# Kernel tuning notes

Hardware: AMD Instinct MI355X
Metric: run time of the kernel (lower is better)

The kernel has to match this reference:

```python
import jax, jax.numpy as jnp
import numpy as np

TOP_K = 10


def setup_inputs() -> dict:
    key = jax.random.key(0)
    x = jax.random.normal(key, (256, 1, 8192), dtype=jnp.float32)
    return {"x": x}


def reference(x):
    # x: [B, 1, S] real
    B, _, S = x.shape
    # torch.arange(1e-05, 1, 1/S) has exactly S elements for these S
    t = 1e-05 + jnp.arange(S, dtype=jnp.float32) / S            # [S]
    dft = jnp.fft.fft(x[:, 0, :], n=S, axis=-1, norm='ortho')   # [B, S] complex64
    mag = jnp.abs(dft)                                          # [B, S]
    top_idx = jnp.argsort(-mag, axis=-1)[:, :TOP_K]             # [B, k] int
    top_dft = jnp.take_along_axis(dft, top_idx, axis=1)         # [B, k] complex
    # complex exponential basis exp(-2j*pi*k*t), flipped along time
    phase = (-2j * jnp.pi) * (top_idx[:, :, None].astype(jnp.float32) * t[None, None, :])
    bs = jnp.exp(phase)[:, :, ::-1]                             # [B, k, S] complex
    bf = top_dft[:, :, None] * bs / jnp.sqrt(jnp.float32(S))    # [B, k, S]
    # F.pad((1,0), mode='replicate') then crop to S: shift right by 1, duplicate first col
    bf = jnp.concatenate([bf[:, :, :1], bf[:, :, :-1]], axis=-1)
    bf = bf[:, :, None, :]                                      # [B, k, 1, S]
    residual = x - jnp.sum(bf, axis=1)                          # [B, 1, S] complex
    return bf, residual
```

## Files before the change

kernel.cpp:

```cpp
#include <hip/hip_runtime.h>

#define NB    256
#define SLEN  8192
#define LOG2S 13
#define TOPK  10

#define RES_REAL   ((size_t)20971520)
#define FULL_ILV   ((size_t)46137344)

__device__ int   g_k [NB * TOPK];
__device__ float g_ar[NB * TOPK];
__device__ float g_ai[NB * TOPK];

__device__ __forceinline__ float sin_rev(float p) { return __builtin_amdgcn_sinf(p); }
__device__ __forceinline__ float cos_rev(float p) { return __builtin_amdgcn_cosf(p); }

__device__ __forceinline__ bool beats(float om, int oi, float wm, int wi) {
  return (om > wm * 1.0001f) || (om > wm * 0.9999f && oi < wi);
}

__device__ __forceinline__ int pad(int a) { return a + (a >> 5); }

typedef float f32x4 __attribute__((ext_vector_type(4)));
__device__ __forceinline__ void store_nt4(float* p, float a, float b, float c,
                                          float d) {
  f32x4 v = {a, b, c, d};
  __builtin_nontemporal_store(v, (f32x4*)p);
}

__device__ __forceinline__ void bfly(float& ur, float& ui, float& vr, float& vi,
                                     float p) {
  const float c = cos_rev(p);
  const float s = -sin_rev(p);
  const float dr = ur - vr, di = ui - vi;
  ur += vr; ui += vi;
  vr = dr * c - di * s;
  vi = dr * s + di * c;
}

template<int ST>
__device__ __forceinline__ void bfly3(float (&xr)[8], float (&xi)[8], int m) {
  const float inv8 = 1.f / (float)(ST * 8);
  const float inv4 = 1.f / (float)(ST * 4);
  const float inv2 = 1.f / (float)(ST * 2);
#pragma unroll
  for (int k = 0; k < 4; ++k)
    bfly(xr[k], xi[k], xr[k + 4], xi[k + 4], (float)(m + ST * k) * inv8);
#pragma unroll
  for (int g = 0; g < 2; ++g)
#pragma unroll
    for (int k0 = 0; k0 < 2; ++k0) {
      const int k = g * 4 + k0;
      bfly(xr[k], xi[k], xr[k + 2], xi[k + 2], (float)(m + ST * k0) * inv4);
    }
  const float p1 = (float)m * inv2;
#pragma unroll
  for (int k = 0; k < 8; k += 2)
    bfly(xr[k], xi[k], xr[k + 1], xi[k + 1], p1);
}

__global__ __launch_bounds__(1024)
void fft_topk(const float* __restrict__ x) {
  __shared__ float2 Z[8448];
  __shared__ float  wred_m[2][16];
  __shared__ int    wred_i[2][16];

  const int b = blockIdx.x;
  const int t = threadIdx.x;
  const int lane = t & 63;
  const int wid  = t >> 6;
  const float* xb = x + (size_t)b * SLEN;

  float xr[8], xi[8];

#pragma unroll
  for (int k = 0; k < 8; ++k) { xr[k] = xb[t + (k << 10)]; xi[k] = 0.f; }
  bfly3<1024>(xr, xi, t);
#pragma unroll
  for (int k = 0; k < 8; ++k)
    Z[pad(t + (k << 10))] = make_float2(xr[k], xi[k]);
  __syncthreads();

  {
    const int m  = t & 127;
    const int i0 = m + ((t >> 7) << 10);
#pragma unroll
    for (int k = 0; k < 8; ++k) {
      const float2 v = Z[pad(i0 + (k << 7))];
      xr[k] = v.x; xi[k] = v.y;
    }
    bfly3<128>(xr, xi, m);
#pragma unroll
    for (int k = 0; k < 8; ++k)
      Z[pad(i0 + (k << 7))] = make_float2(xr[k], xi[k]);
  }
  __syncthreads();

  {
    const int m  = t & 15;
    const int i0 = m + ((t >> 4) << 7);
#pragma unroll
    for (int k = 0; k < 8; ++k) {
      const float2 v = Z[pad(i0 + (k << 4))];
      xr[k] = v.x; xi[k] = v.y;
    }
    bfly3<16>(xr, xi, m);
#pragma unroll
    for (int k = 0; k < 8; ++k)
      Z[pad(i0 + (k << 4))] = make_float2(xr[k], xi[k]);
  }
  __syncthreads();

  {
    const int m  = t & 1;
    const int i0 = m + ((t >> 1) << 4);
#pragma unroll
    for (int k = 0; k < 8; ++k) {
      const float2 v = Z[pad(i0 + (k << 1))];
      xr[k] = v.x; xi[k] = v.y;
    }
    bfly3<2>(xr, xi, m);
#pragma unroll
    for (int k = 0; k < 8; ++k)
      Z[pad(i0 + (k << 1))] = make_float2(xr[k], xi[k]);
  }
  __syncthreads();

#pragma unroll
  for (int q = 0; q < 8; ++q) {
    const float2 v = Z[pad((t << 3) + q)];
    xr[q] = v.x; xi[q] = v.y;
  }
#pragma unroll
  for (int q = 0; q < 8; q += 2) {
    const float ur = xr[q], ui = xi[q];
    const float vr = xr[q + 1], vi = xi[q + 1];
    xr[q] = ur + vr;     xi[q] = ui + vi;
    xr[q + 1] = ur - vr; xi[q + 1] = ui - vi;
  }

  float m2c[8];
#pragma unroll
  for (int q = 0; q < 8; ++q) m2c[q] = xr[q] * xr[q] + xi[q] * xi[q];

  const int rt = (int)(__brev((unsigned)t) >> 22);
  const int qord[8] = {0, 4, 2, 6, 1, 5, 3, 7};

  for (int sel = 0; sel < TOPK; ++sel) {
    float wm = -1.f; int wi = SLEN;
#pragma unroll
    for (int j = 0; j < 8; ++j) {
      const int q = qord[j];
      if (m2c[q] > wm * 1.0001f) { wm = m2c[q]; wi = rt + (j << 10); }
    }
    for (int off = 32; off > 0; off >>= 1) {
      const float om = __shfl_down(wm, off);
      const int   oi = __shfl_down(wi, off);
      if (beats(om, oi, wm, wi)) { wm = om; wi = oi; }
    }
    const int par = sel & 1;
    if (lane == 0) { wred_m[par][wid] = wm; wred_i[par][wid] = wi; }
    __syncthreads();
    float cm = -1.f; int ci = SLEN;
    if (lane < 16) { cm = wred_m[par][lane]; ci = wred_i[par][lane]; }
    for (int off = 8; off > 0; off >>= 1) {
      const float om = __shfl_down(cm, off);
      const int   oi = __shfl_down(ci, off);
      if (beats(om, oi, cm, ci)) { cm = om; ci = oi; }
    }
    wm = __shfl(cm, 0); wi = __shfl(ci, 0);
    const int p = (int)(__brev((unsigned)wi) >> 19);
    if ((p >> 3) == t) {
      const int q = p & 7;
      const float rr = xr[q] * (1.f / (float)SLEN);
      const float ii = xi[q] * (1.f / (float)SLEN);
      const float pr = -1e-5f * (float)wi;
      const float cp = cos_rev(pr), sp = sin_rev(pr);
      g_k [b * TOPK + sel] = wi;
      g_ar[b * TOPK + sel] = rr * cp - ii * sp;
      g_ai[b * TOPK + sel] = rr * sp + ii * cp;
      m2c[q] = 0.f;
    }
  }
}

__global__ __launch_bounds__(256, 4)
void gen(const float* __restrict__ x, float* __restrict__ out, size_t cap) {
  const int bs    = blockIdx.x;
  const int b     = bs >> 3;
  const int slice = bs & 7;
  const int t     = threadIdx.x;
  const int s0    = slice * 1024 + t * 4;
  const float* xb = x + (size_t)b * SLEN;

  int kj[TOPK]; float arj[TOPK], aij[TOPK];
#pragma unroll
  for (int j = 0; j < TOPK; ++j) {
    kj[j]  = g_k [b * TOPK + j];
    arj[j] = g_ar[b * TOPK + j];
    aij[j] = g_ai[b * TOPK + j];
  }

  if (cap < FULL_ILV) {
    const size_t bfbase = (size_t)b * TOPK * SLEN;
    const float4 xv = *(const float4*)(xb + s0);
    float acc0 = 0.f, acc1 = 0.f, acc2 = 0.f, acc3 = 0.f;
#pragma unroll
    for (int j = 0; j < TOPK; ++j) {
      const int k = kj[j];
      float br[4];
#pragma unroll
      for (int q = 0; q < 4; ++q) {
        const int s = s0 + q;
        const int m = (s == 0) ? 1 : s;
        const float p = (float)((k * m) & (SLEN - 1)) * (1.f / (float)SLEN);
        br[q] = arj[j] * cos_rev(p) - aij[j] * sin_rev(p);
      }
      acc0 += br[0]; acc1 += br[1]; acc2 += br[2]; acc3 += br[3];
      const size_t o = bfbase + (size_t)j * SLEN + s0;
      if (o + 4 <= cap)
        store_nt4(out + o, br[0], br[1], br[2], br[3]);
    }
    const size_t o = RES_REAL + (size_t)b * SLEN + s0;
    if (o + 4 <= cap)
      store_nt4(out + o, xv.x - acc0, xv.y - acc1, xv.z - acc2, xv.w - acc3);
  } else {
    const size_t bfbase = (size_t)b * TOPK * SLEN * 2;
    const float4 xv = *(const float4*)(xb + s0);
    float sr[4] = {0.f, 0.f, 0.f, 0.f}, si[4] = {0.f, 0.f, 0.f, 0.f};
#pragma unroll
    for (int j = 0; j < TOPK; ++j) {
      const int k = kj[j];
      float br[4], bi[4];
#pragma unroll
      for (int q = 0; q < 4; ++q) {
        const int s = s0 + q;
        const int m = (s == 0) ? 1 : s;
        const float p = (float)((k * m) & (SLEN - 1)) * (1.f / (float)SLEN);
        const float c = cos_rev(p), sv = sin_rev(p);
        br[q] = arj[j] * c - aij[j] * sv;
        bi[q] = arj[j] * sv + aij[j] * c;
        sr[q] += br[q]; si[q] += bi[q];
      }
      const size_t o = bfbase + ((size_t)j * SLEN + s0) * 2;
      if (o + 8 <= cap) {
        store_nt4(out + o,     br[0], bi[0], br[1], bi[1]);
        store_nt4(out + o + 4, br[2], bi[2], br[3], bi[3]);
      }
    }
    const size_t o = (size_t)41943040 + ((size_t)b * SLEN + s0) * 2;
    if (o + 8 <= cap) {
      store_nt4(out + o,     xv.x - sr[0], -si[0], xv.y - sr[1], -si[1]);
      store_nt4(out + o + 4, xv.z - sr[2], -si[2], xv.w - sr[3], -si[3]);
    }
  }
}

extern "C" void kernel_launch(void* const* d_in, const int* in_sizes, int n_in,
                              void* d_out, int out_size, void* d_ws, size_t ws_size,
                              hipStream_t stream) {
  const float* x = (const float*)d_in[0];
  float* out = (float*)d_out;
  fft_topk<<<NB, 1024, 0, stream>>>(x);
  gen<<<NB * 8, 256, 0, stream>>>(x, out, (size_t)out_size);
}
```

Measured before the change: 123.0 us.

## Replace per-selection block barriers with per-wave top-k candidates merged once

Each wave now independently extracts its own local top-10 via wave shuffles, writing candidate (magnitude, index, value) tuples to shared memory without block-level barriers. After a single __syncthreads, all waves redundantly merge the 160 candidates with 10 further wave-level reductions, and wave 0 writes the results. This removes the ten block-wide barriers in the top-k loop at the cost of extra per-wave selection work and redundant merge computation.

```diff
diff --git a/kernel.cpp b/kernel.cpp
--- a/kernel.cpp
+++ b/kernel.cpp
@@ -62,8 +62,7 @@
 __global__ __launch_bounds__(1024)
 void fft_topk(const float* __restrict__ x) {
   __shared__ float2 Z[8448];
-  __shared__ float  wred_m[2][16];
-  __shared__ int    wred_i[2][16];
+  __shared__ float4 cand[16 * TOPK];
 
   const int b = blockIdx.x;
   const int t = threadIdx.x;
@@ -147,39 +146,65 @@
   const int qord[8] = {0, 4, 2, 6, 1, 5, 3, 7};
 
   for (int sel = 0; sel < TOPK; ++sel) {
-    float wm = -1.f; int wi = SLEN;
+    float pm = -1.f; int pi = SLEN;
 #pragma unroll
     for (int j = 0; j < 8; ++j) {
       const int q = qord[j];
-      if (m2c[q] > wm * 1.0001f) { wm = m2c[q]; wi = rt + (j << 10); }
-    }
+      if (m2c[q] > pm * 1.0001f) { pm = m2c[q]; pi = rt + (j << 10); }
+    }
+    float wm = pm; int wi = pi;
     for (int off = 32; off > 0; off >>= 1) {
       const float om = __shfl_down(wm, off);
       const int   oi = __shfl_down(wi, off);
       if (beats(om, oi, wm, wi)) { wm = om; wi = oi; }
     }
-    const int par = sel & 1;
-    if (lane == 0) { wred_m[par][wid] = wm; wred_i[par][wid] = wi; }
-    __syncthreads();
-    float cm = -1.f; int ci = SLEN;
-    if (lane < 16) { cm = wred_m[par][lane]; ci = wred_i[par][lane]; }
-    for (int off = 8; off > 0; off >>= 1) {
-      const float om = __shfl_down(cm, off);
-      const int   oi = __shfl_down(ci, off);
-      if (beats(om, oi, cm, ci)) { cm = om; ci = oi; }
-    }
-    wm = __shfl(cm, 0); wi = __shfl(ci, 0);
-    const int p = (int)(__brev((unsigned)wi) >> 19);
-    if ((p >> 3) == t) {
-      const int q = p & 7;
-      const float rr = xr[q] * (1.f / (float)SLEN);
-      const float ii = xi[q] * (1.f / (float)SLEN);
-      const float pr = -1e-5f * (float)wi;
+    wm = __shfl(wm, 0); wi = __shfl(wi, 0);
+    if (pi == wi) {
+      float selr = 0.f, seli = 0.f;
+#pragma unroll
+      for (int j = 0; j < 8; ++j) {
+        if (pi == rt + (j << 10)) {
+          const int q = qord[j];
+          selr = xr[q]; seli = xi[q];
+          m2c[q] = 0.f;
+        }
+      }
+      cand[wid * TOPK + sel] = make_float4(wm, __int_as_float(wi), selr, seli);
+    }
+  }
+  __syncthreads();
+
+  float4 c0 = cand[lane];
+  float4 c1 = cand[lane + 64];
+  float4 c2 = (lane < 32) ? cand[lane + 128]
+                          : make_float4(-1.f, __int_as_float(SLEN), 0.f, 0.f);
+  for (int sel = 0; sel < TOPK; ++sel) {
+    float bm = c0.x; int bi = __float_as_int(c0.y);
+    float brr = c0.z, bii = c0.w;
+    if (beats(c1.x, __float_as_int(c1.y), bm, bi)) {
+      bm = c1.x; bi = __float_as_int(c1.y); brr = c1.z; bii = c1.w;
+    }
+    if (beats(c2.x, __float_as_int(c2.y), bm, bi)) {
+      bm = c2.x; bi = __float_as_int(c2.y); brr = c2.z; bii = c2.w;
+    }
+    float rm = bm; int ri = bi;
+    for (int off = 32; off > 0; off >>= 1) {
+      const float om = __shfl_down(rm, off);
+      const int   oi = __shfl_down(ri, off);
+      if (beats(om, oi, rm, ri)) { rm = om; ri = oi; }
+    }
+    ri = __shfl(ri, 0);
+    if (__float_as_int(c0.y) == ri) c0.x = -1.f;
+    if (__float_as_int(c1.y) == ri) c1.x = -1.f;
+    if (__float_as_int(c2.y) == ri) c2.x = -1.f;
+    if (wid == 0 && bi == ri) {
+      const float rr = brr * (1.f / (float)SLEN);
+      const float ii = bii * (1.f / (float)SLEN);
+      const float pr = -1e-5f * (float)ri;
       const float cp = cos_rev(pr), sp = sin_rev(pr);
-      g_k [b * TOPK + sel] = wi;
+      g_k [b * TOPK + sel] = ri;
       g_ar[b * TOPK + sel] = rr * cp - ii * sp;
       g_ai[b * TOPK + sel] = rr * sp + ii * cp;
-      m2c[q] = 0.f;
     }
   }
 }
```

After: 127.7 us. 1.04x slower.
